# Kernel optimization log

Hardware: AMD Instinct MI355X
Metric: run time of the kernel (lower is better)

The kernel has to match this reference:

```python
import jax, jax.numpy as jnp
import numpy as np

N = 100000   # nodes
E = 1600000  # edges (avg degree 16)
M = 20000    # target nodes
D = 128      # input_dim
H = 128      # hidden_dim
H2 = 128     # hidden_dim2
H3 = 64      # hidden_dim3
EPS = 1e-5


def _lin(k, fin, fout, bias=True):
    lim = 1.0 / np.sqrt(fin)
    kw, kb = jax.random.split(k)
    W = jax.random.uniform(kw, (fout, fin), jnp.float32, -lim, lim)
    if bias:
        b = jax.random.uniform(kb, (fout,), jnp.float32, -lim, lim)
        return W, b
    return W


def setup_inputs() -> dict:
    key = jax.random.key(0)
    ks = jax.random.split(key, 16)
    x = jax.random.normal(ks[0], (N, D), jnp.float32)
    edge_index = jax.random.randint(ks[1], (2, E), 0, N, dtype=jnp.int32)
    node_index = jax.random.randint(ks[2], (M,), 0, N, dtype=jnp.int32)
    W1l, b1 = _lin(ks[3], D, H)          # SAGEConv1: lin_l (neighbors, has bias)
    W1r = _lin(ks[4], D, H, bias=False)  # lin_r (root, no bias)
    W2l, b2 = _lin(ks[5], H, H)
    W2r = _lin(ks[6], H, H, bias=False)
    fcW1, fcb1 = _lin(ks[7], H, H2)
    fcW2, fcb2 = _lin(ks[8], H2, H3)
    fcW3, fcb3 = _lin(ks[9], H3, 1)
    g1 = jnp.ones((H2,), jnp.float32); be1 = jnp.zeros((H2,), jnp.float32)
    g2 = jnp.ones((H3,), jnp.float32); be2 = jnp.zeros((H3,), jnp.float32)
    return dict(x=x, edge_index=edge_index, node_index=node_index,
                W1l=W1l, b1=b1, W1r=W1r, W2l=W2l, b2=b2, W2r=W2r,
                fcW1=fcW1, fcb1=fcb1, fcW2=fcW2, fcb2=fcb2, fcW3=fcW3, fcb3=fcb3,
                g1=g1, be1=be1, g2=g2, be2=be2)


def _sage(h, src, dst, Wl, bl, Wr):
    # PyG SAGEConv(aggr='mean'): out = lin_l(mean_{j in N(i)} x_j) + lin_r(x_i)
    msg = h[src]                                                   # [E, F] gather
    s = jax.ops.segment_sum(msg, dst, num_segments=N)              # [N, F]
    cnt = jax.ops.segment_sum(jnp.ones((src.shape[0],), h.dtype), dst, num_segments=N)
    agg = s / jnp.maximum(cnt, 1.0)[:, None]                       # mean, 0 if no nbrs
    return agg @ Wl.T + bl + h @ Wr.T


def _bn(h, g, b):
    # BatchNorm1d training mode: biased batch stats
    mu = jnp.mean(h, axis=0)
    var = jnp.mean(jnp.square(h - mu), axis=0)
    return (h - mu) * jax.lax.rsqrt(var + EPS) * g + b


def reference(x, edge_index, node_index, W1l, b1, W1r, W2l, b2, W2r,
              fcW1, fcb1, fcW2, fcb2, fcW3, fcb3, g1, be1, g2, be2):
    src, dst = edge_index[0], edge_index[1]
    h = jax.nn.relu(_sage(x, src, dst, W1l, b1, W1r))
    h = _sage(h, src, dst, W2l, b2, W2r)
    h = h[node_index]                       # [M, H]
    h = h @ fcW1.T + fcb1
    h = jnp.where(_bn(h, g1, be1) >= 0, _bn(h, g1, be1), 0.1 * _bn(h, g1, be1)) if False else jax.nn.leaky_relu(_bn(h, g1, be1), 0.1)
    h = h @ fcW2.T + fcb2
    h = jax.nn.leaky_relu(_bn(h, g2, be2), 0.05)
    return h @ fcW3.T + fcb3                # [M, 1]
```

## Files before the change

kernel.cpp:

```cpp
#include <hip/hip_runtime.h>
#include <hip/hip_bf16.h>

#define EPSV 1e-5f
#define SEG 512

typedef __attribute__((ext_vector_type(8))) short s16x8;
typedef __attribute__((ext_vector_type(4))) float f32x4;

static __device__ __forceinline__ unsigned short f2b(float f) {
    __hip_bfloat16 h = __float2bfloat16(f);
    return *reinterpret_cast<unsigned short*>(&h);
}


__global__ void k_count_i(const int* __restrict__ dst, int* __restrict__ cnt, int E) {
    int e = blockIdx.x * blockDim.x + threadIdx.x;
    if (e < E) atomicAdd(&cnt[dst[e]], 1);
}

__global__ void k_bsum(const int* __restrict__ cnt, int* __restrict__ bsum, int n) {
    __shared__ int ls[256];
    int t = threadIdx.x;
    int base = blockIdx.x * SEG;
    int v = 0;
    int i0 = base + t, i1 = base + 256 + t;
    if (i0 < n) v += cnt[i0];
    if (i1 < n) v += cnt[i1];
    ls[t] = v;
    __syncthreads();
    for (int off = 128; off > 0; off >>= 1) {
        if (t < off) ls[t] += ls[t + off];
        __syncthreads();
    }
    if (t == 0) bsum[blockIdx.x] = ls[0];
}

__global__ void k_scanb(int* __restrict__ bsum, int B) {
    __shared__ int ls[256];
    int t = threadIdx.x;
    int v = (t < B) ? bsum[t] : 0;
    ls[t] = v;
    __syncthreads();
    for (int off = 1; off < 256; off <<= 1) {
        int u = (t >= off) ? ls[t - off] : 0;
        __syncthreads();
        ls[t] += u;
        __syncthreads();
    }
    if (t < B) bsum[t] = ls[t] - v;
}

__global__ void k_scanseg(const int* __restrict__ cnt, const int* __restrict__ boff,
                          int* __restrict__ rowptr, int* __restrict__ cursor,
                          float* __restrict__ invc, int n, int B) {
    __shared__ int ls[256];
    int t = threadIdx.x;
    int base = blockIdx.x * SEG;
    int i0 = base + 2 * t, i1 = i0 + 1;
    int c0 = (i0 < n) ? cnt[i0] : 0;
    int c1 = (i1 < n) ? cnt[i1] : 0;
    int ts = c0 + c1;
    ls[t] = ts;
    __syncthreads();
    for (int off = 1; off < 256; off <<= 1) {
        int u = (t >= off) ? ls[t - off] : 0;
        __syncthreads();
        ls[t] += u;
        __syncthreads();
    }
    int ex = ls[t] - ts;
    int gb = boff[blockIdx.x];
    int p0 = gb + ex, p1 = p0 + c0;
    if (i0 < n) {
        rowptr[i0] = p0; cursor[i0] = p0;
        invc[i0] = 1.0f / fmaxf((float)c0, 1.0f);
    }
    if (i1 < n) {
        rowptr[i1] = p1; cursor[i1] = p1;
        invc[i1] = 1.0f / fmaxf((float)c1, 1.0f);
    }
    if (blockIdx.x == B - 1 && t == 255) rowptr[n] = gb + ls[255];
}

__global__ void k_fill(const int* __restrict__ src, const int* __restrict__ dst,
                       int* __restrict__ cursor, int* __restrict__ srclist, int E) {
    int e = blockIdx.x * blockDim.x + threadIdx.x;
    if (e < E) {
        int d = dst[e];
        int pos = atomicAdd(&cursor[d], 1);
        srclist[pos] = src[e];
    }
}

__global__ void k_mark(const int* __restrict__ nidx, int* __restrict__ mark,
                       int* __restrict__ list, int* __restrict__ nmarked, int M) {
    int m = blockIdx.x * blockDim.x + threadIdx.x;
    if (m < M) {
        int n = nidx[m];
        if (atomicExch(&mark[n], 1) == 0) list[atomicAdd(nmarked, 1)] = n;
    }
}


__global__ void k_tobf16(const float* __restrict__ in, unsigned short* __restrict__ out, int n4) {
    int i = blockIdx.x * blockDim.x + threadIdx.x;
    int stride = gridDim.x * blockDim.x;
    for (; i < n4; i += stride) {
        float4 v = ((const float4*)in)[i];
        ushort4 u;
        u.x = f2b(v.x); u.y = f2b(v.y); u.z = f2b(v.z); u.w = f2b(v.w);
        ((ushort4*)out)[i] = u;
    }
}

__global__ void k_wconv(const float* __restrict__ W1l, const float* __restrict__ W1r,
                        const float* __restrict__ W2l, const float* __restrict__ W2r,
                        const float* __restrict__ fcW1, const float* __restrict__ fcW2,
                        unsigned short* __restrict__ Wb) {
    int i = blockIdx.x * blockDim.x + threadIdx.x;
    if (i >= 90112) return;
    float v;
    if (i < 16384) v = W1l[i];
    else if (i < 32768) v = W1r[i - 16384];
    else if (i < 49152) v = W2l[i - 32768];
    else if (i < 65536) v = W2r[i - 49152];
    else if (i < 81920) v = fcW1[i - 65536];
    else v = fcW2[i - 81920];
    Wb[i] = f2b(v);
}

__global__ void k_aggr_b(const int* __restrict__ rowptr, const int* __restrict__ srclist,
                         const unsigned int* __restrict__ feat, const float* __restrict__ invc,
                         const int* __restrict__ list, const int* __restrict__ nlist,
                         unsigned int* __restrict__ outf, int n) {
    int lane = threadIdx.x & 63;
    int w = blockIdx.x * (blockDim.x >> 6) + (threadIdx.x >> 6);
    int node;
    if (list) {
        int nm = *nlist;
        if (w >= nm) return;
        node = list[w];
    } else {
        if (w >= n) return;
        node = w;
    }
    int beg = rowptr[node], end = rowptr[node + 1];
    float a0 = 0.f, a1 = 0.f;
    int i = beg;
    for (; i + 4 <= end; i += 4) {
        unsigned u0 = feat[(size_t)srclist[i] * 64 + lane];
        unsigned u1 = feat[(size_t)srclist[i + 1] * 64 + lane];
        unsigned u2 = feat[(size_t)srclist[i + 2] * 64 + lane];
        unsigned u3 = feat[(size_t)srclist[i + 3] * 64 + lane];
        a0 += __uint_as_float(u0 << 16) + __uint_as_float(u1 << 16) +
              __uint_as_float(u2 << 16) + __uint_as_float(u3 << 16);
        a1 += __uint_as_float(u0 & 0xffff0000u) + __uint_as_float(u1 & 0xffff0000u) +
              __uint_as_float(u2 & 0xffff0000u) + __uint_as_float(u3 & 0xffff0000u);
    }
    for (; i < end; i++) {
        unsigned u = feat[(size_t)srclist[i] * 64 + lane];
        a0 += __uint_as_float(u << 16);
        a1 += __uint_as_float(u & 0xffff0000u);
    }
    float ic = invc[node];
    a0 *= ic; a1 *= ic;
    outf[(size_t)node * 64 + lane] = ((unsigned)f2b(a1) << 16) | (unsigned)f2b(a0);
}

template <int NCT, int TWO, int RELU, int OUTBF>
__global__ void k_mdense(const unsigned short* __restrict__ A,
                         const unsigned short* __restrict__ X,
                         const int* __restrict__ gidx,
                         const unsigned short* __restrict__ Wl,
                         const float* __restrict__ bl,
                         const unsigned short* __restrict__ Wr,
                         void* __restrict__ outp, int nrows) {
    const int OC = NCT * 16;
    int lane = threadIdx.x & 63;
    int wave = threadIdx.x >> 6;
    int rowBase = (blockIdx.x * 4 + wave) * 32;
    if (rowBase >= nrows) return;
    int rl = lane & 15;
    int ks = lane >> 4;
    int r0 = rowBase + rl, r1 = r0 + 16;
    int n0 = gidx ? gidx[r0] : r0;
    int n1 = gidx ? gidx[r1] : r1;
    f32x4 acc0[NCT], acc1[NCT];
#pragma unroll
    for (int ct = 0; ct < NCT; ct++) {
        acc0[ct] = (f32x4)0.f;
        acc1[ct] = (f32x4)0.f;
    }
#pragma unroll
    for (int pass = 0; pass < (TWO ? 2 : 1); pass++) {
        const unsigned short* Ain = pass ? X : A;
        const unsigned short* W = pass ? Wr : Wl;
        const s16x8* a0p = (const s16x8*)(Ain + (size_t)n0 * 128);
        const s16x8* a1p = (const s16x8*)(Ain + (size_t)n1 * 128);
#pragma unroll
        for (int kc = 0; kc < 4; kc++) {
            s16x8 af0 = a0p[kc * 4 + ks];
            s16x8 af1 = a1p[kc * 4 + ks];
#pragma unroll
            for (int ct = 0; ct < NCT; ct++) {
                const s16x8* bp = (const s16x8*)(W + (size_t)(ct * 16 + rl) * 128);
                s16x8 bf = bp[kc * 4 + ks];
                acc0[ct] = __builtin_amdgcn_mfma_f32_16x16x32_bf16(af0, bf, acc0[ct], 0, 0, 0);
                acc1[ct] = __builtin_amdgcn_mfma_f32_16x16x32_bf16(af1, bf, acc1[ct], 0, 0, 0);
            }
        }
    }
#pragma unroll
    for (int ct = 0; ct < NCT; ct++) {
        int col = ct * 16 + rl;
        float bj = bl[col];
#pragma unroll
        for (int j = 0; j < 4; j++) {
            int or0 = rowBase + ks * 4 + j;
            int or1 = or0 + 16;
            float v0 = acc0[ct][j] + bj;
            float v1 = acc1[ct][j] + bj;
            if (RELU) { v0 = fmaxf(v0, 0.f); v1 = fmaxf(v1, 0.f); }
            if (OUTBF) {
                ((unsigned short*)outp)[(size_t)or0 * OC + col] = f2b(v0);
                ((unsigned short*)outp)[(size_t)or1 * OC + col] = f2b(v1);
            } else {
                ((float*)outp)[(size_t)or0 * OC + col] = v0;
                ((float*)outp)[(size_t)or1 * OC + col] = v1;
            }
        }
    }
}

template <int C>
__global__ void k_bnstats(const float* __restrict__ z, float* __restrict__ gsum,
                          float* __restrict__ gsq, int nrows, int rowsPerBlock) {
    int t = threadIdx.x;
    int c = t % C;
    int g = t / C;
    const int G = 256 / C;
    int r0 = blockIdx.x * rowsPerBlock;
    int r1 = min(r0 + rowsPerBlock, nrows);
    float s = 0.f, q = 0.f;
    for (int r = r0 + g; r < r1; r += G) {
        float v = z[(size_t)r * C + c];
        s += v;
        q += v * v;
    }
    __shared__ float ls[256], lq[256];
    ls[t] = s;
    lq[t] = q;
    __syncthreads();
    if (t < C) {
        for (int g2 = 1; g2 < G; g2++) {
            s += ls[g2 * C + c];
            q += lq[g2 * C + c];
        }
        atomicAdd(&gsum[c], s);
        atomicAdd(&gsq[c], q);
    }
}

__global__ void k_bnprep(const float* __restrict__ gsum, const float* __restrict__ gsq,
                         const float* __restrict__ gamma, const float* __restrict__ beta,
                         float* __restrict__ scale, float* __restrict__ shift, int C, float invM) {
    int c = blockIdx.x * blockDim.x + threadIdx.x;
    if (c < C) {
        float mean = gsum[c] * invM;
        float var = gsq[c] * invM - mean * mean;
        float is = rsqrtf(var + EPSV);
        float sc = gamma[c] * is;
        scale[c] = sc;
        shift[c] = beta[c] - mean * sc;
    }
}

template <int OUTBF>
__global__ void k_bn_act(const float* __restrict__ z, const float* __restrict__ scale,
                         const float* __restrict__ shift, void* __restrict__ outp,
                         int total, int colsMask, float slope) {
    int i = blockIdx.x * blockDim.x + threadIdx.x;
    if (i < total) {
        int c = i & colsMask;
        float y = z[i] * scale[c] + shift[c];
        y = (y >= 0.f) ? y : slope * y;
        if (OUTBF) ((unsigned short*)outp)[i] = f2b(y);
        else ((float*)outp)[i] = y;
    }
}

__global__ void k_fc3(const float* __restrict__ z2, const float* __restrict__ w,
                      const float* __restrict__ b, float* __restrict__ out, int nrows) {
    int lane = threadIdx.x & 63;
    int m = blockIdx.x * (blockDim.x >> 6) + (threadIdx.x >> 6);
    if (m >= nrows) return;
    float v = z2[(size_t)m * 64 + lane] * w[lane];
    for (int off = 32; off > 0; off >>= 1) v += __shfl_down(v, off);
    if (lane == 0) out[m] = v + b[0];
}

extern "C" void kernel_launch(void* const* d_in, const int* in_sizes, int n_in,
                              void* d_out, int out_size, void* d_ws, size_t ws_size,
                              hipStream_t stream) {
    const float* x    = (const float*)d_in[0];
    const int*   ei   = (const int*)d_in[1];
    const int*   nidx = (const int*)d_in[2];
    const float* W1l  = (const float*)d_in[3];
    const float* b1   = (const float*)d_in[4];
    const float* W1r  = (const float*)d_in[5];
    const float* W2l  = (const float*)d_in[6];
    const float* b2   = (const float*)d_in[7];
    const float* W2r  = (const float*)d_in[8];
    const float* fcW1 = (const float*)d_in[9];
    const float* fcb1 = (const float*)d_in[10];
    const float* fcW2 = (const float*)d_in[11];
    const float* fcb2 = (const float*)d_in[12];
    const float* fcW3 = (const float*)d_in[13];
    const float* fcb3 = (const float*)d_in[14];
    const float* g1   = (const float*)d_in[15];
    const float* be1  = (const float*)d_in[16];
    const float* g2   = (const float*)d_in[17];
    const float* be2  = (const float*)d_in[18];

    const int N = in_sizes[0] / 128;
    const int E = in_sizes[1] / 2;
    const int M = in_sizes[2];
    const int* src = ei;
    const int* dst = ei + E;
    const int B = (N + SEG - 1) / SEG;

    char* ws = (char*)d_ws;
    size_t off = 0;
    unsigned short* xb  = (unsigned short*)(ws + off); off += (size_t)N * 128 * 2;
    unsigned short* sb  = (unsigned short*)(ws + off); off += (size_t)N * 128 * 2;
    unsigned short* h1b = (unsigned short*)(ws + off); off += (size_t)N * 128 * 2;
    unsigned short* z0b = (unsigned short*)(ws + off); off += (size_t)M * 128 * 2;
    float* z1           = (float*)(ws + off);          off += (size_t)M * 128 * 4;
    unsigned short* z1b = (unsigned short*)(ws + off); off += (size_t)M * 128 * 2;
    float* z2           = (float*)(ws + off);          off += (size_t)M * 64 * 4;
    unsigned short* Wb  = (unsigned short*)(ws + off); off += 90112 * 2;
    int*   cnt     = (int*)(ws + off);   off += (size_t)N * 4;
    float* invc    = (float*)(ws + off); off += (size_t)N * 4;
    int*   mark    = (int*)(ws + off);   off += (size_t)N * 4;
    int*   rowptr  = (int*)(ws + off);   off += (size_t)(N + 1) * 4;
    int*   cursor  = (int*)(ws + off);   off += (size_t)N * 4;
    int*   srclist = (int*)(ws + off);   off += (size_t)E * 4;
    int*   list    = (int*)(ws + off);   off += (size_t)M * 4;
    int*   bsum    = (int*)(ws + off);   off += 256 * 4;
    int*   nmarked = (int*)(ws + off);   off += 64;
    float* gsum1   = (float*)(ws + off); off += 128 * 4;
    float* gsq1    = (float*)(ws + off); off += 128 * 4;
    float* scale1  = (float*)(ws + off); off += 128 * 4;
    float* shift1  = (float*)(ws + off); off += 128 * 4;
    float* gsum2   = (float*)(ws + off); off += 64 * 4;
    float* gsq2    = (float*)(ws + off); off += 64 * 4;
    float* scale2  = (float*)(ws + off); off += 64 * 4;
    float* shift2  = (float*)(ws + off); off += 64 * 4;
    float* out = (float*)d_out;

    hipMemsetAsync(cnt, 0, (size_t)N * 4, stream);
    hipMemsetAsync(mark, 0, (size_t)N * 4, stream);
    hipMemsetAsync(nmarked, 0, 4, stream);
    hipMemsetAsync(gsum1, 0, (128 + 128 + 128 + 128 + 64 + 64 + 64 + 64) * 4, stream);

    k_wconv<<<(90112 + 255) / 256, 256, 0, stream>>>(W1l, W1r, W2l, W2r, fcW1, fcW2, Wb);
    k_tobf16<<<2048, 256, 0, stream>>>(x, xb, N * 128 / 4);

    k_count_i<<<(E + 255) / 256, 256, 0, stream>>>(dst, cnt, E);
    k_bsum<<<B, 256, 0, stream>>>(cnt, bsum, N);
    k_scanb<<<1, 256, 0, stream>>>(bsum, B);
    k_scanseg<<<B, 256, 0, stream>>>(cnt, bsum, rowptr, cursor, invc, N, B);
    k_fill<<<(E + 255) / 256, 256, 0, stream>>>(src, dst, cursor, srclist, E);
    k_mark<<<(M + 255) / 256, 256, 0, stream>>>(nidx, mark, list, nmarked, M);

    k_aggr_b<<<(N + 3) / 4, 256, 0, stream>>>(rowptr, srclist, (const unsigned int*)xb, invc,
                                              nullptr, nullptr, (unsigned int*)sb, N);
    k_mdense<8, 1, 1, 1><<<(N / 32 + 3) / 4, 256, 0, stream>>>(
        sb, xb, nullptr, Wb + 0, b1, Wb + 16384, h1b, N);

    k_aggr_b<<<(M + 3) / 4, 256, 0, stream>>>(rowptr, srclist, (const unsigned int*)h1b, invc,
                                              list, nmarked, (unsigned int*)sb, N);
    k_mdense<8, 1, 0, 1><<<(M / 32 + 3) / 4, 256, 0, stream>>>(
        sb, h1b, nidx, Wb + 32768, b2, Wb + 49152, z0b, M);

    k_mdense<8, 0, 0, 0><<<(M / 32 + 3) / 4, 256, 0, stream>>>(
        z0b, nullptr, nullptr, Wb + 65536, fcb1, nullptr, z1, M);
    k_bnstats<128><<<(M + 99) / 100, 256, 0, stream>>>(z1, gsum1, gsq1, M, 100);
    k_bnprep<<<1, 128, 0, stream>>>(gsum1, gsq1, g1, be1, scale1, shift1, 128, 1.0f / M);
    k_bn_act<1><<<((size_t)M * 128 + 255) / 256, 256, 0, stream>>>(
        z1, scale1, shift1, z1b, M * 128, 127, 0.1f);

    k_mdense<4, 0, 0, 0><<<(M / 32 + 3) / 4, 256, 0, stream>>>(
        z1b, nullptr, nullptr, Wb + 81920, fcb2, nullptr, z2, M);
    k_bnstats<64><<<(M + 99) / 100, 256, 0, stream>>>(z2, gsum2, gsq2, M, 100);
    k_bnprep<<<1, 64, 0, stream>>>(gsum2, gsq2, g2, be2, scale2, shift2, 64, 1.0f / M);
    k_bn_act<0><<<((size_t)M * 64 + 255) / 256, 256, 0, stream>>>(
        z2, scale2, shift2, z2, M * 64, 63, 0.05f);

    k_fc3<<<(M + 3) / 4, 256, 0, stream>>>(z2, fcW3, fcb3, out, M);
}
```

Measured before the change: 556.7 us.

## Build CSR via two-level binning with shared-memory atomics

Replaces the global-atomic count, three-kernel scan and atomic scatter fill with a two-level build. Edges are first binned by dst>>7 into fixed-capacity per-bucket buffers, with src and the low dst bits packed into one word. Per-bucket kernels then count, scan and scatter using shared-memory atomics. This is meant to cut contention on global atomics and make the srclist scatter more local. The cost is a large temp buffer and a hard per-bucket capacity of 4096 edges, which random inputs (about 2048 edges per bucket on average) are unlikely to exceed.

```diff
diff --git a/kernel.cpp b/kernel.cpp
--- a/kernel.cpp
+++ b/kernel.cpp
@@ -2,7 +2,7 @@
 #include <hip/hip_bf16.h>
 
 #define EPSV 1e-5f
-#define SEG 512
+#define BCAP 4096
 
 typedef __attribute__((ext_vector_type(8))) short s16x8;
 typedef __attribute__((ext_vector_type(4))) float f32x4;
@@ -13,33 +13,45 @@
 }
 
 
-__global__ void k_count_i(const int* __restrict__ dst, int* __restrict__ cnt, int E) {
+__global__ void k_bin(const int* __restrict__ src, const int* __restrict__ dst,
+                      int* __restrict__ bcur, unsigned* __restrict__ tmp, int E) {
     int e = blockIdx.x * blockDim.x + threadIdx.x;
-    if (e < E) atomicAdd(&cnt[dst[e]], 1);
-}
-
-__global__ void k_bsum(const int* __restrict__ cnt, int* __restrict__ bsum, int n) {
+    if (e < E) {
+        int d = dst[e];
+        int b = d >> 7;
+        int pos = atomicAdd(&bcur[b], 1);
+        tmp[(size_t)b * BCAP + pos] = ((unsigned)src[e] << 7) | (unsigned)(d & 127);
+    }
+}
+
+__global__ void k_bcount(const int* __restrict__ bcur, const unsigned* __restrict__ tmp,
+                         int* __restrict__ cnt, int n) {
+    __shared__ int lc[128];
+    int b = blockIdx.x, t = threadIdx.x;
+    if (t < 128) lc[t] = 0;
+    __syncthreads();
+    int cb = bcur[b];
+    const unsigned* tb = tmp + (size_t)b * BCAP;
+    for (int i = t; i < cb; i += 256) atomicAdd(&lc[tb[i] & 127], 1);
+    __syncthreads();
+    int node = b * 128 + t;
+    if (t < 128 && node < n) cnt[node] = lc[t];
+}
+
+__global__ void k_scanb2(const int* __restrict__ bcur, int* __restrict__ boff, int NB) {
     __shared__ int ls[256];
     int t = threadIdx.x;
-    int base = blockIdx.x * SEG;
-    int v = 0;
-    int i0 = base + t, i1 = base + 256 + t;
-    if (i0 < n) v += cnt[i0];
-    if (i1 < n) v += cnt[i1];
-    ls[t] = v;
-    __syncthreads();
-    for (int off = 128; off > 0; off >>= 1) {
-        if (t < off) ls[t] += ls[t + off];
-        __syncthreads();
-    }
-    if (t == 0) bsum[blockIdx.x] = ls[0];
-}
-
-__global__ void k_scanb(int* __restrict__ bsum, int B) {
-    __shared__ int ls[256];
-    int t = threadIdx.x;
-    int v = (t < B) ? bsum[t] : 0;
-    ls[t] = v;
+    int c = (NB + 255) / 256;
+    int base = t * c;
+    int myv[8];
+    int s = 0;
+    for (int i = 0; i < c; i++) {
+        int idx = base + i;
+        int v = (idx < NB) ? bcur[idx] : 0;
+        myv[i] = v;
+        s += v;
+    }
+    ls[t] = s;
     __syncthreads();
     for (int off = 1; off < 256; off <<= 1) {
         int u = (t >= off) ? ls[t - off] : 0;
@@ -47,48 +59,51 @@
         ls[t] += u;
         __syncthreads();
     }
-    if (t < B) bsum[t] = ls[t] - v;
-}
-
-__global__ void k_scanseg(const int* __restrict__ cnt, const int* __restrict__ boff,
-                          int* __restrict__ rowptr, int* __restrict__ cursor,
-                          float* __restrict__ invc, int n, int B) {
-    __shared__ int ls[256];
-    int t = threadIdx.x;
-    int base = blockIdx.x * SEG;
-    int i0 = base + 2 * t, i1 = i0 + 1;
-    int c0 = (i0 < n) ? cnt[i0] : 0;
-    int c1 = (i1 < n) ? cnt[i1] : 0;
-    int ts = c0 + c1;
-    ls[t] = ts;
-    __syncthreads();
-    for (int off = 1; off < 256; off <<= 1) {
+    int run = ls[t] - s;
+    for (int i = 0; i < c; i++) {
+        int idx = base + i;
+        if (idx < NB) boff[idx] = run;
+        run += myv[i];
+    }
+}
+
+__global__ void k_rowptr(const int* __restrict__ cnt, const int* __restrict__ boff,
+                         int* __restrict__ rowptr, float* __restrict__ invc, int n, int NB) {
+    __shared__ int ls[128];
+    int b = blockIdx.x, t = threadIdx.x;
+    int node = b * 128 + t;
+    int c = (node < n) ? cnt[node] : 0;
+    ls[t] = c;
+    __syncthreads();
+    for (int off = 1; off < 128; off <<= 1) {
         int u = (t >= off) ? ls[t - off] : 0;
         __syncthreads();
         ls[t] += u;
         __syncthreads();
     }
-    int ex = ls[t] - ts;
-    int gb = boff[blockIdx.x];
-    int p0 = gb + ex, p1 = p0 + c0;
-    if (i0 < n) {
-        rowptr[i0] = p0; cursor[i0] = p0;
-        invc[i0] = 1.0f / fmaxf((float)c0, 1.0f);
-    }
-    if (i1 < n) {
-        rowptr[i1] = p1; cursor[i1] = p1;
-        invc[i1] = 1.0f / fmaxf((float)c1, 1.0f);
-    }
-    if (blockIdx.x == B - 1 && t == 255) rowptr[n] = gb + ls[255];
-}
-
-__global__ void k_fill(const int* __restrict__ src, const int* __restrict__ dst,
-                       int* __restrict__ cursor, int* __restrict__ srclist, int E) {
-    int e = blockIdx.x * blockDim.x + threadIdx.x;
-    if (e < E) {
-        int d = dst[e];
-        int pos = atomicAdd(&cursor[d], 1);
-        srclist[pos] = src[e];
+    int ex = ls[t] - c + boff[b];
+    if (node < n) {
+        rowptr[node] = ex;
+        invc[node] = 1.0f / fmaxf((float)c, 1.0f);
+    }
+    if (b == NB - 1 && t == 127) rowptr[n] = boff[b] + ls[127];
+}
+
+__global__ void k_scat2(const int* __restrict__ bcur, const unsigned* __restrict__ tmp,
+                        const int* __restrict__ rowptr, int* __restrict__ srclist, int n) {
+    __shared__ int cur[128];
+    int b = blockIdx.x, t = threadIdx.x;
+    if (t < 128) {
+        int node = b * 128 + t;
+        cur[t] = (node < n) ? rowptr[node] : 0;
+    }
+    __syncthreads();
+    int cb = bcur[b];
+    const unsigned* tb = tmp + (size_t)b * BCAP;
+    for (int i = t; i < cb; i += 256) {
+        unsigned v = tb[i];
+        int pos = atomicAdd(&cur[v & 127], 1);
+        srclist[pos] = (int)(v >> 7);
     }
 }
 
@@ -327,7 +342,7 @@
     const int M = in_sizes[2];
     const int* src = ei;
     const int* dst = ei + E;
-    const int B = (N + SEG - 1) / SEG;
+    const int NB = (N + 127) / 128;
 
     char* ws = (char*)d_ws;
     size_t off = 0;
@@ -339,14 +354,15 @@
     unsigned short* z1b = (unsigned short*)(ws + off); off += (size_t)M * 128 * 2;
     float* z2           = (float*)(ws + off);          off += (size_t)M * 64 * 4;
     unsigned short* Wb  = (unsigned short*)(ws + off); off += 90112 * 2;
+    unsigned* tmp  = (unsigned*)(ws + off); off += (size_t)NB * BCAP * 4;
+    int*   bcur    = (int*)(ws + off);   off += (size_t)NB * 4;
+    int*   boff    = (int*)(ws + off);   off += (size_t)NB * 4;
     int*   cnt     = (int*)(ws + off);   off += (size_t)N * 4;
     float* invc    = (float*)(ws + off); off += (size_t)N * 4;
     int*   mark    = (int*)(ws + off);   off += (size_t)N * 4;
     int*   rowptr  = (int*)(ws + off);   off += (size_t)(N + 1) * 4;
-    int*   cursor  = (int*)(ws + off);   off += (size_t)N * 4;
     int*   srclist = (int*)(ws + off);   off += (size_t)E * 4;
     int*   list    = (int*)(ws + off);   off += (size_t)M * 4;
-    int*   bsum    = (int*)(ws + off);   off += 256 * 4;
     int*   nmarked = (int*)(ws + off);   off += 64;
     float* gsum1   = (float*)(ws + off); off += 128 * 4;
     float* gsq1    = (float*)(ws + off); off += 128 * 4;
@@ -358,7 +374,7 @@
     float* shift2  = (float*)(ws + off); off += 64 * 4;
     float* out = (float*)d_out;
 
-    hipMemsetAsync(cnt, 0, (size_t)N * 4, stream);
+    hipMemsetAsync(bcur, 0, (size_t)NB * 4, stream);
     hipMemsetAsync(mark, 0, (size_t)N * 4, stream);
     hipMemsetAsync(nmarked, 0, 4, stream);
     hipMemsetAsync(gsum1, 0, (128 + 128 + 128 + 128 + 64 + 64 + 64 + 64) * 4, stream);
@@ -366,11 +382,11 @@
     k_wconv<<<(90112 + 255) / 256, 256, 0, stream>>>(W1l, W1r, W2l, W2r, fcW1, fcW2, Wb);
     k_tobf16<<<2048, 256, 0, stream>>>(x, xb, N * 128 / 4);
 
-    k_count_i<<<(E + 255) / 256, 256, 0, stream>>>(dst, cnt, E);
-    k_bsum<<<B, 256, 0, stream>>>(cnt, bsum, N);
-    k_scanb<<<1, 256, 0, stream>>>(bsum, B);
-    k_scanseg<<<B, 256, 0, stream>>>(cnt, bsum, rowptr, cursor, invc, N, B);
-    k_fill<<<(E + 255) / 256, 256, 0, stream>>>(src, dst, cursor, srclist, E);
+    k_bin<<<(E + 255) / 256, 256, 0, stream>>>(src, dst, bcur, tmp, E);
+    k_bcount<<<NB, 256, 0, stream>>>(bcur, tmp, cnt, N);
+    k_scanb2<<<1, 256, 0, stream>>>(bcur, boff, NB);
+    k_rowptr<<<NB, 128, 0, stream>>>(cnt, boff, rowptr, invc, N, NB);
+    k_scat2<<<NB, 256, 0, stream>>>(bcur, tmp, rowptr, srclist, N);
     k_mark<<<(M + 255) / 256, 256, 0, stream>>>(nidx, mark, list, nmarked, M);
 
     k_aggr_b<<<(N + 3) / 4, 256, 0, stream>>>(rowptr, srclist, (const unsigned int*)xb, invc,
```

Measured after the change: 761.4 us. 36.8% more time.

## Replace CSR build with atomic linked lists and pointer-chasing aggregation

Applied to the files above, without the earlier changes.

Removes the count/scan/fill CSR construction and instead builds per-destination linked lists with atomicExch on a head array, storing (next, src) pairs per edge. Aggregation walks these lists, interleaving four nodes per wave to hide dependent-load latency, and computes the mean divisor from the walked count. This cuts several preprocessing kernels and the scan, but turns neighbor traversal into serial dependent random loads that limit memory-level parallelism.

```diff
diff --git a/kernel.cpp b/kernel.cpp
--- a/kernel.cpp
+++ b/kernel.cpp
@@ -2,7 +2,6 @@
 #include <hip/hip_bf16.h>
 
 #define EPSV 1e-5f
-#define SEG 512
 
 typedef __attribute__((ext_vector_type(8))) short s16x8;
 typedef __attribute__((ext_vector_type(4))) float f32x4;
@@ -13,82 +12,12 @@
 }
 
 
-__global__ void k_count_i(const int* __restrict__ dst, int* __restrict__ cnt, int E) {
-    int e = blockIdx.x * blockDim.x + threadIdx.x;
-    if (e < E) atomicAdd(&cnt[dst[e]], 1);
-}
-
-__global__ void k_bsum(const int* __restrict__ cnt, int* __restrict__ bsum, int n) {
-    __shared__ int ls[256];
-    int t = threadIdx.x;
-    int base = blockIdx.x * SEG;
-    int v = 0;
-    int i0 = base + t, i1 = base + 256 + t;
-    if (i0 < n) v += cnt[i0];
-    if (i1 < n) v += cnt[i1];
-    ls[t] = v;
-    __syncthreads();
-    for (int off = 128; off > 0; off >>= 1) {
-        if (t < off) ls[t] += ls[t + off];
-        __syncthreads();
-    }
-    if (t == 0) bsum[blockIdx.x] = ls[0];
-}
-
-__global__ void k_scanb(int* __restrict__ bsum, int B) {
-    __shared__ int ls[256];
-    int t = threadIdx.x;
-    int v = (t < B) ? bsum[t] : 0;
-    ls[t] = v;
-    __syncthreads();
-    for (int off = 1; off < 256; off <<= 1) {
-        int u = (t >= off) ? ls[t - off] : 0;
-        __syncthreads();
-        ls[t] += u;
-        __syncthreads();
-    }
-    if (t < B) bsum[t] = ls[t] - v;
-}
-
-__global__ void k_scanseg(const int* __restrict__ cnt, const int* __restrict__ boff,
-                          int* __restrict__ rowptr, int* __restrict__ cursor,
-                          float* __restrict__ invc, int n, int B) {
-    __shared__ int ls[256];
-    int t = threadIdx.x;
-    int base = blockIdx.x * SEG;
-    int i0 = base + 2 * t, i1 = i0 + 1;
-    int c0 = (i0 < n) ? cnt[i0] : 0;
-    int c1 = (i1 < n) ? cnt[i1] : 0;
-    int ts = c0 + c1;
-    ls[t] = ts;
-    __syncthreads();
-    for (int off = 1; off < 256; off <<= 1) {
-        int u = (t >= off) ? ls[t - off] : 0;
-        __syncthreads();
-        ls[t] += u;
-        __syncthreads();
-    }
-    int ex = ls[t] - ts;
-    int gb = boff[blockIdx.x];
-    int p0 = gb + ex, p1 = p0 + c0;
-    if (i0 < n) {
-        rowptr[i0] = p0; cursor[i0] = p0;
-        invc[i0] = 1.0f / fmaxf((float)c0, 1.0f);
-    }
-    if (i1 < n) {
-        rowptr[i1] = p1; cursor[i1] = p1;
-        invc[i1] = 1.0f / fmaxf((float)c1, 1.0f);
-    }
-    if (blockIdx.x == B - 1 && t == 255) rowptr[n] = gb + ls[255];
-}
-
-__global__ void k_fill(const int* __restrict__ src, const int* __restrict__ dst,
-                       int* __restrict__ cursor, int* __restrict__ srclist, int E) {
+__global__ void k_link(const int* __restrict__ src, const int* __restrict__ dst,
+                       int* __restrict__ head, int2* __restrict__ pk, int E) {
     int e = blockIdx.x * blockDim.x + threadIdx.x;
     if (e < E) {
-        int d = dst[e];
-        int pos = atomicAdd(&cursor[d], 1);
-        srclist[pos] = src[e];
+        int h = atomicExch(&head[dst[e]], e);
+        pk[e] = make_int2(h, src[e]);
     }
 }
 
@@ -129,42 +58,44 @@
     Wb[i] = f2b(v);
 }
 
-__global__ void k_aggr_b(const int* __restrict__ rowptr, const int* __restrict__ srclist,
-                         const unsigned int* __restrict__ feat, const float* __restrict__ invc,
-                         const int* __restrict__ list, const int* __restrict__ nlist,
-                         unsigned int* __restrict__ outf, int n) {
+__global__ void k_aggr_chase(const int* __restrict__ head, const int2* __restrict__ pk,
+                             const unsigned* __restrict__ feat,
+                             const int* __restrict__ list, const int* __restrict__ nlist,
+                             unsigned* __restrict__ outf, int n) {
     int lane = threadIdx.x & 63;
     int w = blockIdx.x * (blockDim.x >> 6) + (threadIdx.x >> 6);
-    int node;
-    if (list) {
-        int nm = *nlist;
-        if (w >= nm) return;
-        node = list[w];
-    } else {
-        if (w >= n) return;
-        node = w;
-    }
-    int beg = rowptr[node], end = rowptr[node + 1];
-    float a0 = 0.f, a1 = 0.f;
-    int i = beg;
-    for (; i + 4 <= end; i += 4) {
-        unsigned u0 = feat[(size_t)srclist[i] * 64 + lane];
-        unsigned u1 = feat[(size_t)srclist[i + 1] * 64 + lane];
-        unsigned u2 = feat[(size_t)srclist[i + 2] * 64 + lane];
-        unsigned u3 = feat[(size_t)srclist[i + 3] * 64 + lane];
-        a0 += __uint_as_float(u0 << 16) + __uint_as_float(u1 << 16) +
-              __uint_as_float(u2 << 16) + __uint_as_float(u3 << 16);
-        a1 += __uint_as_float(u0 & 0xffff0000u) + __uint_as_float(u1 & 0xffff0000u) +
-              __uint_as_float(u2 & 0xffff0000u) + __uint_as_float(u3 & 0xffff0000u);
-    }
-    for (; i < end; i++) {
-        unsigned u = feat[(size_t)srclist[i] * 64 + lane];
-        a0 += __uint_as_float(u << 16);
-        a1 += __uint_as_float(u & 0xffff0000u);
-    }
-    float ic = invc[node];
-    a0 *= ic; a1 *= ic;
-    outf[(size_t)node * 64 + lane] = ((unsigned)f2b(a1) << 16) | (unsigned)f2b(a0);
+    int limit = list ? *nlist : n;
+    int node[4], e[4], cnt[4];
+    float a0[4], a1[4];
+#pragma unroll
+    for (int c = 0; c < 4; c++) {
+        int idx = w * 4 + c;
+        node[c] = (idx < limit) ? (list ? list[idx] : idx) : -1;
+        e[c] = (node[c] >= 0) ? head[node[c]] : -1;
+        a0[c] = 0.f; a1[c] = 0.f; cnt[c] = 0;
+    }
+    while (e[0] >= 0 || e[1] >= 0 || e[2] >= 0 || e[3] >= 0) {
+#pragma unroll
+        for (int c = 0; c < 4; c++) {
+            if (e[c] >= 0) {
+                int2 p = pk[e[c]];
+                unsigned u = feat[(size_t)p.y * 64 + lane];
+                a0[c] += __uint_as_float(u << 16);
+                a1[c] += __uint_as_float(u & 0xffff0000u);
+                cnt[c]++;
+                e[c] = p.x;
+            }
+        }
+    }
+#pragma unroll
+    for (int c = 0; c < 4; c++) {
+        if (node[c] >= 0) {
+            float ic = 1.0f / fmaxf((float)cnt[c], 1.0f);
+            float v0 = a0[c] * ic, v1 = a1[c] * ic;
+            outf[(size_t)node[c] * 64 + lane] =
+                ((unsigned)f2b(v1) << 16) | (unsigned)f2b(v0);
+        }
+    }
 }
 
 template <int NCT, int TWO, int RELU, int OUTBF>
@@ -327,7 +258,6 @@
     const int M = in_sizes[2];
     const int* src = ei;
     const int* dst = ei + E;
-    const int B = (N + SEG - 1) / SEG;
 
     char* ws = (char*)d_ws;
     size_t off = 0;
@@ -339,15 +269,11 @@
     unsigned short* z1b = (unsigned short*)(ws + off); off += (size_t)M * 128 * 2;
     float* z2           = (float*)(ws + off);          off += (size_t)M * 64 * 4;
     unsigned short* Wb  = (unsigned short*)(ws + off); off += 90112 * 2;
-    int*   cnt     = (int*)(ws + off);   off += (size_t)N * 4;
-    float* invc    = (float*)(ws + off); off += (size_t)N * 4;
-    int*   mark    = (int*)(ws + off);   off += (size_t)N * 4;
-    int*   rowptr  = (int*)(ws + off);   off += (size_t)(N + 1) * 4;
-    int*   cursor  = (int*)(ws + off);   off += (size_t)N * 4;
-    int*   srclist = (int*)(ws + off);   off += (size_t)E * 4;
-    int*   list    = (int*)(ws + off);   off += (size_t)M * 4;
-    int*   bsum    = (int*)(ws + off);   off += 256 * 4;
-    int*   nmarked = (int*)(ws + off);   off += 64;
+    int2* pk       = (int2*)(ws + off);  off += (size_t)E * 8;
+    int*  head     = (int*)(ws + off);   off += (size_t)N * 4;
+    int*  mark     = (int*)(ws + off);   off += (size_t)N * 4;
+    int*  list     = (int*)(ws + off);   off += (size_t)M * 4;
+    int*  nmarked  = (int*)(ws + off);   off += 64;
     float* gsum1   = (float*)(ws + off); off += 128 * 4;
     float* gsq1    = (float*)(ws + off); off += 128 * 4;
     float* scale1  = (float*)(ws + off); off += 128 * 4;
@@ -358,7 +284,7 @@
     float* shift2  = (float*)(ws + off); off += 64 * 4;
     float* out = (float*)d_out;
 
-    hipMemsetAsync(cnt, 0, (size_t)N * 4, stream);
+    hipMemsetAsync(head, 0xFF, (size_t)N * 4, stream);
     hipMemsetAsync(mark, 0, (size_t)N * 4, stream);
     hipMemsetAsync(nmarked, 0, 4, stream);
     hipMemsetAsync(gsum1, 0, (128 + 128 + 128 + 128 + 64 + 64 + 64 + 64) * 4, stream);
@@ -366,20 +292,22 @@
     k_wconv<<<(90112 + 255) / 256, 256, 0, stream>>>(W1l, W1r, W2l, W2r, fcW1, fcW2, Wb);
     k_tobf16<<<2048, 256, 0, stream>>>(x, xb, N * 128 / 4);
 
-    k_count_i<<<(E + 255) / 256, 256, 0, stream>>>(dst, cnt, E);
-    k_bsum<<<B, 256, 0, stream>>>(cnt, bsum, N);
-    k_scanb<<<1, 256, 0, stream>>>(bsum, B);
-    k_scanseg<<<B, 256, 0, stream>>>(cnt, bsum, rowptr, cursor, invc, N, B);
-    k_fill<<<(E + 255) / 256, 256, 0, stream>>>(src, dst, cursor, srclist, E);
+    k_link<<<(E + 255) / 256, 256, 0, stream>>>(src, dst, head, pk, E);
     k_mark<<<(M + 255) / 256, 256, 0, stream>>>(nidx, mark, list, nmarked, M);
 
-    k_aggr_b<<<(N + 3) / 4, 256, 0, stream>>>(rowptr, srclist, (const unsigned int*)xb, invc,
-                                              nullptr, nullptr, (unsigned int*)sb, N);
+    {
+        int waves = (N + 3) / 4;
+        k_aggr_chase<<<(waves + 3) / 4, 256, 0, stream>>>(
+            head, pk, (const unsigned*)xb, nullptr, nullptr, (unsigned*)sb, N);
+    }
     k_mdense<8, 1, 1, 1><<<(N / 32 + 3) / 4, 256, 0, stream>>>(
         sb, xb, nullptr, Wb + 0, b1, Wb + 16384, h1b, N);
 
-    k_aggr_b<<<(M + 3) / 4, 256, 0, stream>>>(rowptr, srclist, (const unsigned int*)h1b, invc,
-                                              list, nmarked, (unsigned int*)sb, N);
+    {
+        int waves = (M + 3) / 4;
+        k_aggr_chase<<<(waves + 3) / 4, 256, 0, stream>>>(
+            head, pk, (const unsigned*)h1b, list, nmarked, (unsigned*)sb, N);
+    }
     k_mdense<8, 1, 0, 1><<<(M / 32 + 3) / 4, 256, 0, stream>>>(
         sb, h1b, nidx, Wb + 32768, b2, Wb + 49152, z0b, M);
 
```

Result: slower. 574.3 us (+3.2%).
